# Optimization experiments

Measured on AMD Instinct MI355X. Metric: run time of the kernel, lower is better.

The kernel has to match this reference:

```python
import jax, jax.numpy as jnp
import numpy as np

N, R, L, H, D, E = 30000, 3, 4, 128, 128, 20000  # nodes, ranks, max group len, hidden, input_dim, n_hyperedges
NUM_HEADS = 4


def _xavier(rng, fan_in, fan_out, shape=None):
    bound = np.sqrt(6.0 / (fan_in + fan_out))
    shape = (fan_in, fan_out) if shape is None else shape
    return jnp.asarray(rng.uniform(-bound, bound, size=shape), dtype=jnp.float32)


def setup_inputs() -> dict:
    rng = np.random.default_rng(0)
    # hyperedge id h has rank h % R; ids of rank r are r + R*k
    deg = 1 + (np.arange(N * R).reshape(N, R) % L)          # per (node, rank) group size in 1..L
    mask = np.arange(L)[None, None, :] < deg[:, :, None]    # [N,R,L] valid slots
    ks = rng.integers(0, E // R, size=(N, R, L))
    he_idx = ks * R + np.arange(R)[None, :, None]           # hyperedge ids matching each rank row
    he_idx = np.where(mask, he_idx, 0)
    valid_idx = np.flatnonzero(mask.reshape(-1)).astype(np.int64)  # [nnz], nnz = 225000
    # he_order: per-node argsort of its (rank-ordered) valid hyperedge id list, plus running offset
    flatm = mask.reshape(N, R * L)
    row_vals = np.where(flatm, he_idx.reshape(N, R * L), E + 1)
    perm = np.argsort(row_vals, axis=1, kind='stable')      # positions of sorted values
    compact = np.cumsum(flatm, axis=1) - 1                   # padded pos -> compact (valid-list) index
    deg_total = flatm.sum(1)
    offsets = np.concatenate([[0], np.cumsum(deg_total)[:-1]])
    compact_at_perm = np.take_along_axis(compact, perm, axis=1)
    take = np.arange(R * L)[None, :] < deg_total[:, None]
    he_order = (compact_at_perm + offsets[:, None])[take].astype(np.int64)
    inp = {
        'x_rank': jnp.asarray(rng.standard_normal((N, R, D)), jnp.float32),
        'he_features': jnp.asarray(rng.standard_normal((E, H)), jnp.float32),
        'he_idx': jnp.asarray(he_idx, jnp.int32),
        'valid_idx': jnp.asarray(valid_idx, jnp.int32),
        'he_order': jnp.asarray(he_order, jnp.int32),
        # GRU gate parameters (whh: hidden->hidden, wxh: input->hidden, b: hidden)
        'r_whh': _xavier(rng, H, H), 'r_wxh': _xavier(rng, D, H), 'r_b': jnp.zeros((H,), jnp.float32),
        'u_whh': _xavier(rng, H, H), 'u_wxh': _xavier(rng, D, H), 'u_b': jnp.zeros((H,), jnp.float32),
        'c_whh': _xavier(rng, H, H), 'c_wxh': _xavier(rng, D, H), 'c_b': jnp.zeros((H,), jnp.float32),
        # MultiheadAttention params (torch layout: in_proj_weight [3H,H])
        'in_proj_w': _xavier(rng, 3 * H, H, shape=(3 * H, H)),
        'in_proj_b': jnp.zeros((3 * H,), jnp.float32),
        'out_w': _xavier(rng, H, H, shape=(H, H)),
        'out_b': jnp.zeros((H,), jnp.float32),
    }
    return inp


def reference(x_rank, he_features, he_idx, valid_idx, he_order,
              r_whh, r_wxh, r_b, u_whh, u_wxh, u_b, c_whh, c_wxh, c_b,
              in_proj_w, in_proj_b, out_w, out_b):
    n, n_ranks, _ = x_rank.shape
    hd = H // NUM_HEADS

    # ---- GRU over ranks (sequence axis) ----
    def step(h, x_t):
        r = jax.nn.sigmoid(h @ r_whh + x_t @ r_wxh + r_b)
        z = jax.nn.sigmoid(h @ u_whh + x_t @ u_wxh + u_b)
        c = jnp.tanh((r * h) @ c_whh + x_t @ c_wxh + c_b)  # (r*h)@W per python precedence
        h = z * c + (1.0 - z) * h
        return h, h

    h0 = jnp.zeros((n, H), x_rank.dtype)
    _, hs = jax.lax.scan(step, h0, jnp.swapaxes(x_rank, 0, 1))  # [R,N,H]
    hs = jnp.swapaxes(hs, 0, 1)                                  # [N,R,H]

    # ---- ragged gather-pad + per (node, rank) MHA with a single key/value ----
    wq, wk, wv = in_proj_w[:H], in_proj_w[H:2 * H], in_proj_w[2 * H:]
    bq, bk, bv = in_proj_b[:H], in_proj_b[H:2 * H], in_proj_b[2 * H:]
    q = he_features[he_idx]                                       # [N,R,L,H]
    qp = (q @ wq.T + bq).reshape(n, n_ranks, L, NUM_HEADS, hd)
    kp = (hs @ wk.T + bk).reshape(n, n_ranks, NUM_HEADS, hd)
    vp = (hs @ wv.T + bv).reshape(n, n_ranks, NUM_HEADS, hd)
    scale = 1.0 / jnp.sqrt(jnp.asarray(hd, q.dtype))
    scores = jnp.einsum('nrlhd,nrhd->nrlh', qp, kp) * scale       # key length is 1
    attn = jax.nn.softmax(scores[..., None], axis=-1)[..., 0]     # softmax over singleton key axis -> 1
    ctx = attn[..., None] * vp[:, :, None]                        # [N,R,L,heads,hd]
    out = ctx.reshape(n, n_ranks, L, H) @ out_w.T + out_b         # [N,R,L,H]
    # select valid (non-padded) slots, concatenated in node/rank order
    result = out.reshape(-1, H)[valid_idx]                        # [nnz,H]
    return result, he_order
```

## Files before the change

kernel.cpp:

```cpp
#include <hip/hip_runtime.h>
#include <math.h>

#define Hd 128
#define Rr 3
#define Ll 4
#define NPW 16
#define NW  8

typedef float f32x4 __attribute__((ext_vector_type(4)));
typedef short s16x8 __attribute__((ext_vector_type(8)));

__device__ __forceinline__ unsigned short f2bf(float f){
    unsigned u = __float_as_uint(f);
    return (unsigned short)((u + 0x7FFFu + ((u >> 16) & 1u)) >> 16);
}
__device__ __forceinline__ s16x8 cvt8(const float* p){
    float4 a = *(const float4*)p;
    float4 b = *(const float4*)(p + 4);
    float v[8] = {a.x, a.y, a.z, a.w, b.x, b.y, b.z, b.w};
    s16x8 r;
    #pragma unroll
    for (int j = 0; j < 8; ++j) r[j] = (short)f2bf(v[j]);
    return r;
}
__device__ __forceinline__ int lower_bound_i32(const int* __restrict__ a, int n, int key){
    int lo = 0, hi = n;
    while (lo < hi){
        int mid = (lo + hi) >> 1;
        if (a[mid] < key) lo = mid + 1; else hi = mid;
    }
    return lo;
}

__device__ __forceinline__ void gload_lds16(const unsigned short* g, unsigned short* l){
    __builtin_amdgcn_global_load_lds(
        (const __attribute__((address_space(1))) void*)g,
        (__attribute__((address_space(3))) void*)l, 16, 0, 0);
}

__global__ void fold_proj_kernel(const float* __restrict__ in_proj_w,
                                 const float* __restrict__ in_proj_b,
                                 const float* __restrict__ out_w,
                                 const float* __restrict__ out_b,
                                 float* __restrict__ McT,
                                 float* __restrict__ bc)
{
    const int i = blockIdx.x;
    const int j = threadIdx.x;
    float acc = 0.f;
    for (int k = 0; k < Hd; ++k)
        acc = fmaf(out_w[j * Hd + k], in_proj_w[(2 * Hd + k) * Hd + i], acc);
    McT[i * Hd + j] = acc;
    if (i == 0){
        float b = out_b[j];
        for (int k = 0; k < Hd; ++k)
            b = fmaf(out_w[j * Hd + k], in_proj_b[2 * Hd + k], b);
        bc[j] = b;
    }
}

__global__ void pack_kernel(const float* __restrict__ r_whh, const float* __restrict__ u_whh,
                            const float* __restrict__ r_wxh, const float* __restrict__ u_wxh,
                            const float* __restrict__ c_whh, const float* __restrict__ c_wxh,
                            const float* __restrict__ McT,
                            unsigned short* __restrict__ whi)
{
    const int mat  = blockIdx.y;
    const int tile = blockIdx.x;
    const int l    = threadIdx.x;
    const float* W;
    switch (mat){
        case 0: W = r_whh; break;  case 1: W = u_whh; break;
        case 2: W = r_wxh; break;  case 3: W = u_wxh; break;
        case 4: W = c_whh; break;  case 5: W = c_wxh; break;
        default: W = McT;
    }
    const int kc = tile >> 3, nc = tile & 7;
    const int kbase = kc * 32 + (l >> 4) * 8;
    const int n = nc * 16 + (l & 15);
    const size_t obase = ((size_t)(mat * 32 + tile) * 64 + l) * 8;
    #pragma unroll
    for (int j = 0; j < 8; ++j)
        whi[obase + j] = f2bf(W[(kbase + j) * Hd + n]);
}

#define BF_LDS(kc, nc) (*(const s16x8*)&WL[cur][(((kc) * 8 + (nc)) * 64 + l) * 8])

#define MM1(acc, AH, BH)                                                  \
    acc = __builtin_amdgcn_mfma_f32_16x16x32_bf16(AH, BH, acc, 0, 0, 0);

__global__ __launch_bounds__(512, 1) void gru_mfma_kernel(
    const float* __restrict__ x_rank,
    const int* __restrict__ valid_idx, int nv,
    const float* __restrict__ r_b, const float* __restrict__ u_b, const float* __restrict__ c_b,
    const unsigned short* __restrict__ whi,
    const float* __restrict__ bc,
    float* __restrict__ out, int N)
{
    __shared__ __align__(16) unsigned short WL[2][16384];
    __shared__ __align__(16) float Sr_all[NW][NPW][132];
    __shared__ float bias_s[4][Hd];
    __shared__ int lo_all[NW][NPW];
    __shared__ int hi_all[NW][NPW];

    const int tid = threadIdx.x;
    const int wid = tid >> 6;
    const int l   = tid & 63;
    const int lr  = l & 15;
    const int lg  = l >> 4;
    const int n0  = (blockIdx.x * NW + wid) * NPW;

    float (*Sr)[132] = Sr_all[wid];
    int* loL = lo_all[wid];
    int* hiL = hi_all[wid];

    if (tid < Hd){
        bias_s[0][tid] = r_b[tid];
        bias_s[1][tid] = u_b[tid];
        bias_s[2][tid] = c_b[tid];
        bias_s[3][tid] = bc[tid];
    }

    #define STAGE_MAT(mat, b)                                                    \
        {                                                                        \
            const unsigned short* msrc = whi + (size_t)(mat) * 16384;            \
            _Pragma("unroll")                                                    \
            for (int it = 0; it < 4; ++it){                                      \
                const int chunk = it * 8 + wid;                                  \
                gload_lds16(msrc + chunk * 512 + l * 8, &WL[b][chunk * 512]);    \
            }                                                                    \
        }

    f32x4 hD[8];
    s16x8 ah[4];
    #pragma unroll
    for (int nc = 0; nc < 8; ++nc) hD[nc] = (f32x4){0.f, 0.f, 0.f, 0.f};
    #pragma unroll
    for (int kc = 0; kc < 4; ++kc) ah[kc] = (s16x8)0;

    s16x8 xh[4], rhh[4];

    unsigned cur = 0;
    STAGE_MAT(0, 0);

    #pragma unroll 1
    for (int t = 0; t < Rr; ++t){
        if (l < NPW){
            int n = n0 + l, lo = 0, hi = 0;
            if (n < N){
                int F = (n * Rr + t) * Ll;
                lo = lower_bound_i32(valid_idx, nv, F);
                hi = lower_bound_i32(valid_idx, nv, F + Ll);
            }
            loL[l] = lo; hiL[l] = hi;
        }

        {
            int nn = n0 + lr; if (nn > N - 1) nn = N - 1;
            const float* xp = x_rank + ((size_t)nn * Rr + t) * Hd;
            #pragma unroll
            for (int kc = 0; kc < 4; ++kc)
                xh[kc] = cvt8(xp + kc * 32 + lg * 8);
        }

        f32x4 accR[8], accZ[8];

        __syncthreads();
        STAGE_MAT(2, cur ^ 1);
        #pragma unroll
        for (int nc = 0; nc < 8; ++nc){
            accR[nc] = (f32x4){0.f, 0.f, 0.f, 0.f};
            #pragma unroll
            for (int kc = 0; kc < 4; ++kc){ s16x8 b = BF_LDS(kc, nc); MM1(accR[nc], ah[kc], b); }
            if ((nc & 3) == 3) __builtin_amdgcn_sched_barrier(0);
        }
        cur ^= 1;

        __syncthreads();
        STAGE_MAT(1, cur ^ 1);
        #pragma unroll
        for (int nc = 0; nc < 8; ++nc){
            #pragma unroll
            for (int kc = 0; kc < 4; ++kc){ s16x8 b = BF_LDS(kc, nc); MM1(accR[nc], xh[kc], b); }
            const float rbc = bias_s[0][nc * 16 + lr];
            #pragma unroll
            for (int i = 0; i < 4; ++i){
                float r = 1.f / (1.f + __expf(-(accR[nc][i] + rbc)));
                Sr[lg * 4 + i][nc * 16 + lr] = r * hD[nc][i];
            }
            if ((nc & 3) == 3) __builtin_amdgcn_sched_barrier(0);
        }
        cur ^= 1;

        __syncthreads();
        STAGE_MAT(3, cur ^ 1);
        #pragma unroll
        for (int nc = 0; nc < 8; ++nc){
            accZ[nc] = (f32x4){0.f, 0.f, 0.f, 0.f};
            #pragma unroll
            for (int kc = 0; kc < 4; ++kc){ s16x8 b = BF_LDS(kc, nc); MM1(accZ[nc], ah[kc], b); }
            if ((nc & 3) == 3) __builtin_amdgcn_sched_barrier(0);
        }
        cur ^= 1;

        __syncthreads();
        STAGE_MAT(4, cur ^ 1);
        #pragma unroll
        for (int nc = 0; nc < 8; ++nc){
            #pragma unroll
            for (int kc = 0; kc < 4; ++kc){ s16x8 b = BF_LDS(kc, nc); MM1(accZ[nc], xh[kc], b); }
            const float ubc = bias_s[1][nc * 16 + lr];
            #pragma unroll
            for (int i = 0; i < 4; ++i)
                accZ[nc][i] = 1.f / (1.f + __expf(-(accZ[nc][i] + ubc)));
            if ((nc & 3) == 3) __builtin_amdgcn_sched_barrier(0);
        }
        cur ^= 1;

        __syncthreads();
        STAGE_MAT(5, cur ^ 1);
        #pragma unroll
        for (int kc = 0; kc < 4; ++kc)
            rhh[kc] = cvt8(&Sr[lr][kc * 32 + lg * 8]);
        f32x4 accC[8];
        #pragma unroll
        for (int nc = 0; nc < 8; ++nc){
            accC[nc] = (f32x4){0.f, 0.f, 0.f, 0.f};
            #pragma unroll
            for (int kc = 0; kc < 4; ++kc){ s16x8 b = BF_LDS(kc, nc); MM1(accC[nc], rhh[kc], b); }
            if ((nc & 3) == 3) __builtin_amdgcn_sched_barrier(0);
        }
        cur ^= 1;

        __syncthreads();
        STAGE_MAT(6, cur ^ 1);
        #pragma unroll
        for (int nc = 0; nc < 8; ++nc){
            #pragma unroll
            for (int kc = 0; kc < 4; ++kc){ s16x8 b = BF_LDS(kc, nc); MM1(accC[nc], xh[kc], b); }
            const float cbc = bias_s[2][nc * 16 + lr];
            #pragma unroll
            for (int i = 0; i < 4; ++i){
                float e = __expf(2.f * (accC[nc][i] + cbc));
                float c = 1.f - 2.f / (e + 1.f);
                float ho = hD[nc][i];
                float hn = ho + accZ[nc][i] * (c - ho);
                hD[nc][i] = hn;
                Sr[lg * 4 + i][nc * 16 + lr] = hn;
            }
            if ((nc & 3) == 3) __builtin_amdgcn_sched_barrier(0);
        }
        #pragma unroll
        for (int kc = 0; kc < 4; ++kc)
            ah[kc] = cvt8(&Sr[lr][kc * 32 + lg * 8]);
        cur ^= 1;

        __syncthreads();
        if (t < Rr - 1) STAGE_MAT(0, cur ^ 1);
        #pragma unroll
        for (int nc = 0; nc < 8; ++nc){
            f32x4 ao = (f32x4){0.f, 0.f, 0.f, 0.f};
            #pragma unroll
            for (int kc = 0; kc < 4; ++kc){ s16x8 b = BF_LDS(kc, nc); MM1(ao, ah[kc], b); }
            const float obc = bias_s[3][nc * 16 + lr];
            #pragma unroll
            for (int i = 0; i < 4; ++i)
                Sr[lg * 4 + i][nc * 16 + lr] = ao[i] + obc;
            if ((nc & 3) == 3) __builtin_amdgcn_sched_barrier(0);
        }
        __builtin_amdgcn_sched_barrier(0);

        #pragma unroll
        for (int m = 0; m < 8; ++m){
            const int row = m * 2 + (l >> 5);
            const int c4  = (l & 31) * 4;
            const float4 v = *(const float4*)&Sr[row][c4];
            const int lo = loL[row], hi = hiL[row];
            for (int rr = lo; rr < hi; ++rr)
                *(float4*)(out + (size_t)rr * Hd + c4) = v;
        }
        cur ^= 1;
    }
    #undef STAGE_MAT
}

__global__ void he_order_kernel(const int* __restrict__ he_order,
                                float* __restrict__ out_tail, int nv)
{
    const int i = blockIdx.x * 256 + threadIdx.x;
    if (i < nv) out_tail[i] = (float)he_order[i];
}

extern "C" void kernel_launch(void* const* d_in, const int* in_sizes, int n_in,
                              void* d_out, int out_size, void* d_ws, size_t ws_size,
                              hipStream_t stream)
{
    const float* x_rank    = (const float*)d_in[0];
    const int*   valid_idx = (const int*)d_in[3];
    const int*   he_order  = (const int*)d_in[4];
    const float* r_whh = (const float*)d_in[5];
    const float* r_wxh = (const float*)d_in[6];
    const float* r_b   = (const float*)d_in[7];
    const float* u_whh = (const float*)d_in[8];
    const float* u_wxh = (const float*)d_in[9];
    const float* u_b   = (const float*)d_in[10];
    const float* c_whh = (const float*)d_in[11];
    const float* c_wxh = (const float*)d_in[12];
    const float* c_b   = (const float*)d_in[13];
    const float* in_proj_w = (const float*)d_in[14];
    const float* in_proj_b = (const float*)d_in[15];
    const float* out_w     = (const float*)d_in[16];
    const float* out_b     = (const float*)d_in[17];

    const int nv = in_sizes[3];
    const int N  = in_sizes[0] / (Rr * Hd);

    float* McT = (float*)d_ws;
    float* bc  = McT + Hd * Hd;
    unsigned short* whi = (unsigned short*)(bc + Hd);

    float* out_f    = (float*)d_out;
    float* out_tail = out_f + (size_t)nv * Hd;

    fold_proj_kernel<<<Hd, Hd, 0, stream>>>(in_proj_w, in_proj_b, out_w, out_b, McT, bc);
    pack_kernel<<<dim3(32, 7), 64, 0, stream>>>(r_whh, u_whh, r_wxh, u_wxh, c_whh, c_wxh,
                                                McT, whi);

    const int nodes_per_block = NW * NPW;
    const int nblocks = (N + nodes_per_block - 1) / nodes_per_block;
    gru_mfma_kernel<<<nblocks, 512, 0, stream>>>(
        x_rank, valid_idx, nv, r_b, u_b, c_b, whi, bc, out_f, N);

    he_order_kernel<<<(nv + 255) / 256, 256, 0, stream>>>(he_order, out_tail, nv);
}
```

Baseline: 97.28 us.

## Precompute input-side GRU gate projections in a separate kernel, trim recurrent kernel

Splits the GRU into a parallel kernel that computes all input-to-hidden gate projections (plus biases) for every rank, stored as bf16 in workspace. A leaner recurrent kernel then does only hidden-to-hidden matmuls: it skips the zero hidden-state matmuls at step 0, fuses the r and z gate matmuls into one phase with three LDS weight buffers, and stores intermediates in bf16 shared memory. This removes serial-chain work and barriers from the recurrent kernel. In exchange it adds a workspace round-trip of the gate projections, extra bf16 rounding, and a fallback path that depends on the workspace size.

Result: slower. 127.1 us (+30.7%).

```diff
diff --git a/kernel.cpp b/kernel.cpp
--- a/kernel.cpp
+++ b/kernel.cpp
@@ -6,6 +6,7 @@
 #define Ll 4
 #define NPW 16
 #define NW  8
+#define SRP 136
 
 typedef float f32x4 __attribute__((ext_vector_type(4)));
 typedef short s16x8 __attribute__((ext_vector_type(8)));
@@ -13,6 +14,9 @@
 __device__ __forceinline__ unsigned short f2bf(float f){
     unsigned u = __float_as_uint(f);
     return (unsigned short)((u + 0x7FFFu + ((u >> 16) & 1u)) >> 16);
+}
+__device__ __forceinline__ float bf2f(unsigned short h){
+    return __uint_as_float(((unsigned)h) << 16);
 }
 __device__ __forceinline__ s16x8 cvt8(const float* p){
     float4 a = *(const float4*)p;
@@ -31,11 +35,14 @@
     }
     return lo;
 }
-
 __device__ __forceinline__ void gload_lds16(const unsigned short* g, unsigned short* l){
     __builtin_amdgcn_global_load_lds(
         (const __attribute__((address_space(1))) void*)g,
         (__attribute__((address_space(3))) void*)l, 16, 0, 0);
+}
+__device__ __forceinline__ float gxel(uint2 u, int i){
+    unsigned w = (i < 2) ? u.x : u.y;
+    return bf2f((unsigned short)((i & 1) ? (w >> 16) : (w & 0xffff)));
 }
 
 __global__ void fold_proj_kernel(const float* __restrict__ in_proj_w,
@@ -84,12 +91,272 @@
         whi[obase + j] = f2bf(W[(kbase + j) * Hd + n]);
 }
 
-#define BF_LDS(kc, nc) (*(const s16x8*)&WL[cur][(((kc) * 8 + (nc)) * 64 + l) * 8])
-
 #define MM1(acc, AH, BH)                                                  \
     acc = __builtin_amdgcn_mfma_f32_16x16x32_bf16(AH, BH, acc, 0, 0, 0);
 
-__global__ __launch_bounds__(512, 1) void gru_mfma_kernel(
+__global__ __launch_bounds__(512, 1) void gx_kernel(
+    const float* __restrict__ x_rank,
+    const float* __restrict__ r_b, const float* __restrict__ u_b, const float* __restrict__ c_b,
+    const unsigned short* __restrict__ whi,
+    uint2* __restrict__ gx, int N, int NT)
+{
+    __shared__ __align__(16) unsigned short WX[2][16384];
+    const int tid = threadIdx.x;
+    const int wid = tid >> 6;
+    const int l   = tid & 63;
+    const int lr  = l & 15;
+    const int lg  = l >> 4;
+
+    #define STAGE_X(mat, b)                                                      \
+        {                                                                        \
+            const unsigned short* msrc = whi + (size_t)(mat) * 16384;            \
+            _Pragma("unroll")                                                    \
+            for (int it = 0; it < 4; ++it){                                      \
+                const int chunk = it * 8 + wid;                                  \
+                gload_lds16(msrc + chunk * 512 + l * 8, &WX[b][chunk * 512]);    \
+            }                                                                    \
+        }
+
+    STAGE_X(2, 0);
+
+    const int u = blockIdx.x * NW + wid;
+    const int valid = (u < 3 * NT);
+    const int uu = valid ? u : 3 * NT - 1;
+    const int t  = uu / NT;
+    const int nt = uu % NT;
+
+    int nn = nt * NPW + lr; if (nn > N - 1) nn = N - 1;
+    const float* xp = x_rank + ((size_t)nn * Rr + t) * Hd;
+    s16x8 xh[4];
+    #pragma unroll
+    for (int kc = 0; kc < 4; ++kc)
+        xh[kc] = cvt8(xp + kc * 32 + lg * 8);
+
+    #define GX_COMP(g, b, bp)                                                    \
+        {                                                                        \
+            _Pragma("unroll")                                                    \
+            for (int nc = 0; nc < 8; ++nc){                                      \
+                f32x4 acc = (f32x4){0.f, 0.f, 0.f, 0.f};                         \
+                _Pragma("unroll")                                                \
+                for (int kc = 0; kc < 4; ++kc){                                  \
+                    s16x8 bb = *(const s16x8*)&WX[b][(((kc) * 8 + nc) * 64 + l) * 8]; \
+                    MM1(acc, xh[kc], bb);                                        \
+                }                                                                \
+                const float bv = bp[nc * 16 + lr];                               \
+                uint2 o;                                                         \
+                o.x = ((unsigned)f2bf(acc[1] + bv) << 16) | f2bf(acc[0] + bv);   \
+                o.y = ((unsigned)f2bf(acc[3] + bv) << 16) | f2bf(acc[2] + bv);   \
+                if (valid)                                                       \
+                    gx[(((size_t)((g) * Rr + t) * NT + nt) * 8 + nc) * 64 + l] = o; \
+                if ((nc & 3) == 3) __builtin_amdgcn_sched_barrier(0);            \
+            }                                                                    \
+        }
+
+    __syncthreads();
+    STAGE_X(3, 1);
+    GX_COMP(0, 0, r_b);
+    __syncthreads();
+    STAGE_X(5, 0);
+    GX_COMP(1, 1, u_b);
+    __syncthreads();
+    GX_COMP(2, 0, c_b);
+    #undef GX_COMP
+    #undef STAGE_X
+}
+
+#define BF3(b, kc, nc) (*(const s16x8*)&WL[b][(((kc) * 8 + (nc)) * 64 + l) * 8])
+#define GXLD(g, t, nc) gx[(((size_t)((g) * Rr + (t)) * NT + gtile) * 8 + (nc)) * 64 + l]
+
+__global__ __launch_bounds__(512, 1) void gru_rec7_kernel(
+    const int* __restrict__ valid_idx, int nv,
+    const unsigned short* __restrict__ whi,
+    const uint2* __restrict__ gx,
+    const float* __restrict__ bc,
+    float* __restrict__ out, int N, int NT)
+{
+    __shared__ __align__(16) unsigned short WL[3][16384];
+    __shared__ __align__(16) unsigned short Sr_all[NW][NPW][SRP];
+    __shared__ int lo_all[NW][NPW];
+    __shared__ int hi_all[NW][NPW];
+
+    const int tid = threadIdx.x;
+    const int wid = tid >> 6;
+    const int l   = tid & 63;
+    const int lr  = l & 15;
+    const int lg  = l >> 4;
+    const int wtile = blockIdx.x * NW + wid;
+    const int n0  = wtile * NPW;
+    const int gtile = (wtile < NT) ? wtile : NT - 1;
+
+    unsigned short (*Sr)[SRP] = Sr_all[wid];
+    int* loL = lo_all[wid];
+    int* hiL = hi_all[wid];
+
+    #define STAGE_MAT(mat, b)                                                    \
+        {                                                                        \
+            const unsigned short* msrc = whi + (size_t)(mat) * 16384;            \
+            _Pragma("unroll")                                                    \
+            for (int it = 0; it < 4; ++it){                                      \
+                const int chunk = it * 8 + wid;                                  \
+                gload_lds16(msrc + chunk * 512 + l * 8, &WL[b][chunk * 512]);    \
+            }                                                                    \
+        }
+
+    #define LOHI(T)                                                              \
+        if (l < NPW){                                                            \
+            int n = n0 + l, lo = 0, hi = 0;                                      \
+            if (n < N){                                                          \
+                int F = (n * Rr + (T)) * Ll;                                     \
+                lo = lower_bound_i32(valid_idx, nv, F);                          \
+                hi = lower_bound_i32(valid_idx, nv, F + Ll);                     \
+            }                                                                    \
+            loL[l] = lo; hiL[l] = hi;                                            \
+        }
+
+    f32x4 hD[8], zD[8];
+    s16x8 ah[4];
+    uint2 gc8[8];
+    float obc[8];
+    #pragma unroll
+    for (int nc = 0; nc < 8; ++nc) obc[nc] = bc[nc * 16 + lr];
+
+    STAGE_MAT(6, 0);
+    STAGE_MAT(0, 1);
+    STAGE_MAT(1, 2);
+
+    LOHI(0)
+    {
+        uint2 gu0[8];
+        #pragma unroll
+        for (int nc = 0; nc < 8; ++nc){ gu0[nc] = GXLD(1, 0, nc); gc8[nc] = GXLD(2, 0, nc); }
+        #pragma unroll
+        for (int nc = 0; nc < 8; ++nc){
+            #pragma unroll
+            for (int i = 0; i < 4; ++i){
+                float z = 1.f / (1.f + __expf(-gxel(gu0[nc], i)));
+                float e = __expf(2.f * gxel(gc8[nc], i));
+                float c = 1.f - 2.f / (e + 1.f);
+                float hn = z * c;
+                hD[nc][i] = hn;
+                Sr[lg * 4 + i][nc * 16 + lr] = f2bf(hn);
+            }
+        }
+        #pragma unroll
+        for (int kc = 0; kc < 4; ++kc)
+            ah[kc] = *(const s16x8*)&Sr[lr][kc * 32 + lg * 8];
+    }
+
+    #define P1_PHASE(T, BR, BZ)                                                  \
+        {                                                                        \
+            LOHI(T)                                                              \
+            uint2 gr[8], gu[8];                                                  \
+            _Pragma("unroll")                                                    \
+            for (int nc = 0; nc < 8; ++nc){                                      \
+                gr[nc] = GXLD(0, T, nc); gu[nc] = GXLD(1, T, nc);                \
+                gc8[nc] = GXLD(2, T, nc);                                        \
+            }                                                                    \
+            _Pragma("unroll")                                                    \
+            for (int nc = 0; nc < 8; ++nc){                                      \
+                f32x4 aR = (f32x4){0.f, 0.f, 0.f, 0.f};                          \
+                f32x4 aZ = (f32x4){0.f, 0.f, 0.f, 0.f};                          \
+                _Pragma("unroll")                                                \
+                for (int kc = 0; kc < 4; ++kc){ s16x8 b = BF3(BR, kc, nc); MM1(aR, ah[kc], b); } \
+                _Pragma("unroll")                                                \
+                for (int kc = 0; kc < 4; ++kc){ s16x8 b = BF3(BZ, kc, nc); MM1(aZ, ah[kc], b); } \
+                _Pragma("unroll")                                                \
+                for (int i = 0; i < 4; ++i){                                     \
+                    float r = 1.f / (1.f + __expf(-(aR[i] + gxel(gr[nc], i))));  \
+                    Sr[lg * 4 + i][nc * 16 + lr] = f2bf(r * hD[nc][i]);          \
+                    zD[nc][i] = 1.f / (1.f + __expf(-(aZ[i] + gxel(gu[nc], i)))); \
+                }                                                                \
+                if (nc & 1) __builtin_amdgcn_sched_barrier(0);                   \
+            }                                                                    \
+        }
+
+    #define P2_PHASE(BC)                                                         \
+        {                                                                        \
+            s16x8 rhh[4];                                                        \
+            _Pragma("unroll")                                                    \
+            for (int kc = 0; kc < 4; ++kc)                                       \
+                rhh[kc] = *(const s16x8*)&Sr[lr][kc * 32 + lg * 8];              \
+            _Pragma("unroll")                                                    \
+            for (int nc = 0; nc < 8; ++nc){                                      \
+                f32x4 aC = (f32x4){0.f, 0.f, 0.f, 0.f};                          \
+                _Pragma("unroll")                                                \
+                for (int kc = 0; kc < 4; ++kc){ s16x8 b = BF3(BC, kc, nc); MM1(aC, rhh[kc], b); } \
+                _Pragma("unroll")                                                \
+                for (int i = 0; i < 4; ++i){                                     \
+                    float e = __expf(2.f * (aC[i] + gxel(gc8[nc], i)));          \
+                    float c = 1.f - 2.f / (e + 1.f);                             \
+                    float ho = hD[nc][i];                                        \
+                    float hn = ho + zD[nc][i] * (c - ho);                        \
+                    hD[nc][i] = hn;                                              \
+                    Sr[lg * 4 + i][nc * 16 + lr] = f2bf(hn);                     \
+                }                                                                \
+                if ((nc & 3) == 3) __builtin_amdgcn_sched_barrier(0);            \
+            }                                                                    \
+            _Pragma("unroll")                                                    \
+            for (int kc = 0; kc < 4; ++kc)                                       \
+                ah[kc] = *(const s16x8*)&Sr[lr][kc * 32 + lg * 8];               \
+        }
+
+    #define O_PHASE(BO)                                                          \
+        {                                                                        \
+            _Pragma("unroll")                                                    \
+            for (int nc = 0; nc < 8; ++nc){                                      \
+                f32x4 ao = (f32x4){0.f, 0.f, 0.f, 0.f};                          \
+                _Pragma("unroll")                                                \
+                for (int kc = 0; kc < 4; ++kc){ s16x8 b = BF3(BO, kc, nc); MM1(ao, ah[kc], b); } \
+                _Pragma("unroll")                                                \
+                for (int i = 0; i < 4; ++i)                                      \
+                    Sr[lg * 4 + i][nc * 16 + lr] = f2bf(ao[i] + obc[nc]);        \
+                if ((nc & 3) == 3) __builtin_amdgcn_sched_barrier(0);            \
+            }                                                                    \
+            _Pragma("unroll")                                                    \
+            for (int m = 0; m < 8; ++m){                                         \
+                const int row = m * 2 + (l >> 5);                                \
+                const int c4  = (l & 31) * 4;                                    \
+                const uint2 u2 = *(const uint2*)&Sr[row][c4];                    \
+                float4 v = { bf2f((unsigned short)(u2.x & 0xffff)),              \
+                             bf2f((unsigned short)(u2.x >> 16)),                 \
+                             bf2f((unsigned short)(u2.y & 0xffff)),              \
+                             bf2f((unsigned short)(u2.y >> 16)) };               \
+                const int lo = loL[row], hi = hiL[row];                          \
+                for (int rr = lo; rr < hi; ++rr)                                 \
+                    *(float4*)(out + (size_t)rr * Hd + c4) = v;                  \
+            }                                                                    \
+        }
+
+    __syncthreads();
+    O_PHASE(0)
+    __syncthreads();
+    STAGE_MAT(4, 0);
+    P1_PHASE(1, 1, 2)
+    __syncthreads();
+    STAGE_MAT(6, 1);
+    P2_PHASE(0)
+    __syncthreads();
+    STAGE_MAT(0, 2);
+    STAGE_MAT(1, 0);
+    O_PHASE(1)
+    __syncthreads();
+    STAGE_MAT(4, 1);
+    P1_PHASE(2, 2, 0)
+    __syncthreads();
+    STAGE_MAT(6, 2);
+    P2_PHASE(1)
+    __syncthreads();
+    O_PHASE(2)
+
+    #undef O_PHASE
+    #undef P2_PHASE
+    #undef P1_PHASE
+    #undef LOHI
+    #undef STAGE_MAT
+}
+
+#define BF_LDS(kc, nc) (*(const s16x8*)&WL[cur][(((kc) * 8 + (nc)) * 64 + l) * 8])
+__global__ __launch_bounds__(512, 1) void gru_mfma_fb(
     const float* __restrict__ x_rank,
     const int* __restrict__ valid_idx, int nv,
     const float* __restrict__ r_b, const float* __restrict__ u_b, const float* __restrict__ c_b,
@@ -120,7 +387,6 @@
         bias_s[2][tid] = c_b[tid];
         bias_s[3][tid] = bc[tid];
     }
-
     #define STAGE_MAT(mat, b)                                                    \
         {                                                                        \
             const unsigned short* msrc = whi + (size_t)(mat) * 16384;            \
@@ -130,14 +396,12 @@
                 gload_lds16(msrc + chunk * 512 + l * 8, &WL[b][chunk * 512]);    \
             }                                                                    \
         }
-
     f32x4 hD[8];
     s16x8 ah[4];
     #pragma unroll
     for (int nc = 0; nc < 8; ++nc) hD[nc] = (f32x4){0.f, 0.f, 0.f, 0.f};
     #pragma unroll
     for (int kc = 0; kc < 4; ++kc) ah[kc] = (s16x8)0;
-
     s16x8 xh[4], rhh[4];
 
     unsigned cur = 0;
@@ -154,7 +418,6 @@
             }
             loL[l] = lo; hiL[l] = hi;
         }
-
         {
             int nn = n0 + lr; if (nn > N - 1) nn = N - 1;
             const float* xp = x_rank + ((size_t)nn * Rr + t) * Hd;
@@ -162,9 +425,7 @@
             for (int kc = 0; kc < 4; ++kc)
                 xh[kc] = cvt8(xp + kc * 32 + lg * 8);
         }
-
         f32x4 accR[8], accZ[8];
-
         __syncthreads();
         STAGE_MAT(2, cur ^ 1);
         #pragma unroll
@@ -175,7 +436,6 @@
             if ((nc & 3) == 3) __builtin_amdgcn_sched_barrier(0);
         }
         cur ^= 1;
-
         __syncthreads();
         STAGE_MAT(1, cur ^ 1);
         #pragma unroll
@@ -191,7 +451,6 @@
             if ((nc & 3) == 3) __builtin_amdgcn_sched_barrier(0);
         }
         cur ^= 1;
-
         __syncthreads();
         STAGE_MAT(3, cur ^ 1);
         #pragma unroll
@@ -202,7 +461,6 @@
             if ((nc & 3) == 3) __builtin_amdgcn_sched_barrier(0);
         }
         cur ^= 1;
-
         __syncthreads();
         STAGE_MAT(4, cur ^ 1);
         #pragma unroll
@@ -216,7 +474,6 @@
             if ((nc & 3) == 3) __builtin_amdgcn_sched_barrier(0);
         }
         cur ^= 1;
-
         __syncthreads();
         STAGE_MAT(5, cur ^ 1);
         #pragma unroll
@@ -231,7 +488,6 @@
             if ((nc & 3) == 3) __builtin_amdgcn_sched_barrier(0);
         }
         cur ^= 1;
-
         __syncthreads();
         STAGE_MAT(6, cur ^ 1);
         #pragma unroll
@@ -254,7 +510,6 @@
         for (int kc = 0; kc < 4; ++kc)
             ah[kc] = cvt8(&Sr[lr][kc * 32 + lg * 8]);
         cur ^= 1;
-
         __syncthreads();
         if (t < Rr - 1) STAGE_MAT(0, cur ^ 1);
         #pragma unroll
@@ -268,8 +523,6 @@
                 Sr[lg * 4 + i][nc * 16 + lr] = ao[i] + obc;
             if ((nc & 3) == 3) __builtin_amdgcn_sched_barrier(0);
         }
-        __builtin_amdgcn_sched_barrier(0);
-
         #pragma unroll
         for (int m = 0; m < 8; ++m){
             const int row = m * 2 + (l >> 5);
@@ -314,10 +567,14 @@
 
     const int nv = in_sizes[3];
     const int N  = in_sizes[0] / (Rr * Hd);
+    const int NT = (N + NPW - 1) / NPW;
 
     float* McT = (float*)d_ws;
     float* bc  = McT + Hd * Hd;
     unsigned short* whi = (unsigned short*)(bc + Hd);
+    const size_t base = 16384*4 + 128*4 + 7*16384*2;
+    uint2* gx = (uint2*)((char*)d_ws + base);
+    const size_t gx_bytes = (size_t)9 * NT * 8 * 64 * 8;
 
     float* out_f    = (float*)d_out;
     float* out_tail = out_f + (size_t)nv * Hd;
@@ -328,8 +585,15 @@
 
     const int nodes_per_block = NW * NPW;
     const int nblocks = (N + nodes_per_block - 1) / nodes_per_block;
-    gru_mfma_kernel<<<nblocks, 512, 0, stream>>>(
-        x_rank, valid_idx, nv, r_b, u_b, c_b, whi, bc, out_f, N);
+
+    if (ws_size >= base + gx_bytes){
+        const int gxblocks = (3 * NT + NW - 1) / NW;
+        gx_kernel<<<gxblocks, 512, 0, stream>>>(x_rank, r_b, u_b, c_b, whi, gx, N, NT);
+        gru_rec7_kernel<<<nblocks, 512, 0, stream>>>(valid_idx, nv, whi, gx, bc, out_f, N, NT);
+    } else {
+        gru_mfma_fb<<<nblocks, 512, 0, stream>>>(
+            x_rank, valid_idx, nv, r_b, u_b, c_b, whi, bc, out_f, N);
+    }
 
     he_order_kernel<<<(nv + 255) / 256, 256, 0, stream>>>(he_order, out_tail, nv);
 }
```
